# Kernel optimization log

Hardware: AMD Instinct MI355X
Metric: run time of the kernel (lower is better)

Reference implementation:

```python
import jax, jax.numpy as jnp
import numpy as np

N_NODES = 50000   # hypergraph nodes
N_EDGES = 20000   # hyperedges
M = 400000        # node-edge incidences (node copies)
L = 800000        # inner GIN graph edges per side
HID = 128
IN_DIM = 128
B = 32            # graphs in batch
C = 10            # num_classes
N_LAYERS = 2
INNER = 2         # inner_num_layers
BN_EPS = 1e-5


def setup_inputs() -> dict:
    key = jax.random.key(0)
    ks = jax.random.split(key, 16)
    s = 0.05
    inp = {}
    inp["x_N"] = jax.random.normal(ks[0], (N_NODES, IN_DIM), jnp.float32)
    # embedding linear
    inp["We"] = jax.random.normal(ks[1], (IN_DIM, HID), jnp.float32) * s
    inp["be"] = jnp.zeros((HID,), jnp.float32)
    # GIN params: [outer_layer, direction(N2E/E2N), inner_conv, mlp_linear, hid, hid]
    inp["Wg"] = jax.random.normal(ks[2], (N_LAYERS, 2, INNER, 2, HID, HID), jnp.float32) * s
    inp["bg"] = jnp.zeros((N_LAYERS, 2, INNER, 2, HID), jnp.float32)
    inp["eps_g"] = jnp.zeros((N_LAYERS, 2, INNER), jnp.float32)
    # eval-mode BatchNorm affine params per inner conv
    inp["gamma"] = jnp.ones((N_LAYERS, 2, INNER, HID), jnp.float32)
    inp["beta"] = jnp.zeros((N_LAYERS, 2, INNER, HID), jnp.float32)
    # per-layer prediction heads
    inp["Wp"] = jax.random.normal(ks[3], (N_LAYERS + 1, HID, C), jnp.float32) * s
    inp["bp"] = jnp.zeros((N_LAYERS + 1, C), jnp.float32)
    # index tensors
    inp["ori_node_idx"] = jax.random.randint(ks[4], (M,), 0, N_NODES)
    inp["node2edge"] = jax.random.randint(ks[5], (M,), 0, N_EDGES)
    inp["edge_index_N"] = jax.random.randint(ks[6], (2, L), 0, M)
    inp["ori_edge_idx"] = jax.random.randint(ks[7], (M,), 0, N_EDGES)
    inp["edge2node"] = jax.random.randint(ks[8], (M,), 0, N_NODES)
    inp["edge_index_E"] = jax.random.randint(ks[9], (2, L), 0, M)
    inp["batch"] = jax.random.randint(ks[10], (M,), 0, B)
    return inp


def _gin(x, src, dst, Wg, bg, eps, gamma, beta):
    # GIN over the copy graph: h = MLP((1+eps)*x + sum_{j->i} x_j), BN (eval), ReLU between convs
    inv_std = 1.0 / jnp.sqrt(1.0 + BN_EPS)
    n = x.shape[0]
    for l in range(INNER):
        agg = jax.ops.segment_sum(x[src], dst, num_segments=n)
        h = (1.0 + eps[l]) * x + agg
        h = jax.nn.relu(h @ Wg[l, 0] + bg[l, 0])
        h = h @ Wg[l, 1] + bg[l, 1]
        h = gamma[l] * h * inv_std + beta[l]
        x = jax.nn.relu(h) if l < INNER - 1 else h
    return x


def reference(x_N, We, be, Wg, bg, eps_g, gamma, beta, Wp, bp,
              ori_node_idx, node2edge, edge_index_N,
              ori_edge_idx, edge2node, edge_index_E, batch):
    node_x = x_N @ We + be                       # [N, HID]
    xs = [node_x]
    for i in range(N_LAYERS):
        # node -> edge: gather copies, inner GIN, segment-sum pool over hyperedges
        nx = node_x[ori_node_idx]                # [M, HID]
        nx = _gin(nx, edge_index_N[0], edge_index_N[1],
                  Wg[i, 0], bg[i, 0], eps_g[i, 0], gamma[i, 0], beta[i, 0])
        edge_x = jax.ops.segment_sum(nx, node2edge, num_segments=N_EDGES)
        edge_x = jax.nn.relu(edge_x)             # EdgeUpdate (dropout off in eval)
        # edge -> node
        ex = edge_x[ori_edge_idx]                # [M, HID]
        ex = _gin(ex, edge_index_E[0], edge_index_E[1],
                  Wg[i, 1], bg[i, 1], eps_g[i, 1], gamma[i, 1], beta[i, 1])
        node_x = jax.ops.segment_sum(ex, edge2node, num_segments=N_NODES)
        node_x = jax.nn.relu(node_x)             # NodeUpdate
        xs.append(node_x)
    score = jnp.zeros((B, C), x_N.dtype)
    for i, x in enumerate(xs):
        pooled = jax.ops.segment_sum(x[ori_node_idx], batch, num_segments=B)
        score = score + pooled @ Wp[i] + bp[i]
    return score
```

## Files before the change

### kernel.cpp

```cpp
#include <hip/hip_runtime.h>
#include <hip/hip_bf16.h>

#define HID 128
static const int N_NODES = 50000;
static const int N_EDGES = 20000;
static const int M_COPIES = 400000;
static const int L_EDGES = 800000;
static const int NBATCH = 32;
static const int NCLS = 10;
#define INV_STD 0.9999950000374997f
#define IDX_CAP 384
#define PKSHIFT 19
#define PKMASK  0x7FFFF

typedef __attribute__((ext_vector_type(4))) float f32x4;
typedef __attribute__((ext_vector_type(8))) short short8;
typedef __attribute__((ext_vector_type(8))) unsigned short ushort8;
typedef __attribute__((ext_vector_type(4))) unsigned short u16x4;

__device__ __forceinline__ float bf2f(unsigned short u) {
    union { unsigned u; float f; } v; v.u = ((unsigned)u) << 16; return v.f;
}
__device__ __forceinline__ unsigned short f2bf(float f) {
    union { float f; unsigned u; } v; v.f = f;
    unsigned r = v.u + 0x7FFFu + ((v.u >> 16) & 1u);
    return (unsigned short)(r >> 16);
}
__device__ __forceinline__ void gatomic_add(float* p, float v) {
    unsafeAtomicAdd(p, v);
}

__device__ __forceinline__ unsigned short* xs_addr(unsigned short* Xs, int c, int r) {
    int byte = ((c * 64 + r) * 16) ^ ((c & 7) << 4);
    return (unsigned short*)((char*)Xs + byte);
}

__device__ __forceinline__ void stage8(const unsigned short* __restrict__ Wmat, int e,
                                       unsigned short* buf, int wave, int lane) {
    const char* g = (const char*)Wmat + ((size_t)e << 12) + (wave << 10) + (lane << 4);
    char* l = (char*)buf + (wave << 10);
    __builtin_amdgcn_global_load_lds(
        (const __attribute__((address_space(1))) unsigned int*)g,
        (__attribute__((address_space(3))) unsigned int*)l,
        16, 0, 0);
}

template<int N>
__device__ __forceinline__ void pipe_barrier() {
    if constexpr (N == 0) asm volatile("s_waitcnt vmcnt(0)" ::: "memory");
    else                  asm volatile("s_waitcnt vmcnt(1)" ::: "memory");
    __builtin_amdgcn_s_barrier();
    asm volatile("" ::: "memory");
}

__device__ __forceinline__ void mfma4(const unsigned short* Ws, const short8* xv,
                                      f32x4& a, int quad, int ln) {
#pragma unroll
    for (int kc = 0; kc < 4; ++kc) {
        short8 wa = *(const short8*)(Ws + (((kc * 4 + quad) * 16) + ln) * 8);
        a = __builtin_amdgcn_mfma_f32_16x16x32_bf16(wa, xv[kc], a, 0, 0, 0);
    }
}

__global__ __launch_bounds__(256) void prep_w(const float* __restrict__ We,
                                              const float* __restrict__ Wg,
                                              unsigned short* __restrict__ Wt) {
    int t = blockIdx.x * 256 + threadIdx.x;
    if (t >= 17 * 16384) return;
    int mat = t >> 14, rem = t & 16383;
    int h = rem >> 11, r2 = rem & 2047;
    int gg = r2 >> 7, r3 = r2 & 127;
    int n = r3 >> 3, j = r3 & 7;
    int k = gg * 8 + j, col = h * 16 + n;
    const float* src = (mat == 0) ? We : (Wg + (size_t)(mat - 1) * 16384);
    Wt[t] = f2bf(src[k * 128 + col]);
}

__global__ __launch_bounds__(256) void hist2_k(
    const int* __restrict__ iA, int nA, int* __restrict__ cA,
    const int* __restrict__ iB, int nB, int* __restrict__ cB, int shift) {
    int t = blockIdx.x * 256 + threadIdx.x;
    if (t < nA) atomicAdd(&cA[iA[t] >> shift], 1);
    if (t < nB) atomicAdd(&cB[iB[t] >> shift], 1);
}

__global__ __launch_bounds__(256) void scan1d_k(
    int* __restrict__ a0, int n0, int* __restrict__ p0,
    int* __restrict__ a1, int n1, int* __restrict__ p1) {
    int* a    = blockIdx.y ? a1 : a0;
    int n     = blockIdx.y ? n1 : n0;
    int* part = blockIdx.y ? p1 : p0;
    if ((int)(blockIdx.x * 256) >= n) return;
    __shared__ int s[256];
    int i = blockIdx.x * 256 + threadIdx.x;
    int v = (i < n) ? a[i] : 0;
    s[threadIdx.x] = v;
    __syncthreads();
#pragma unroll
    for (int d = 1; d < 256; d <<= 1) {
        int t = (threadIdx.x >= d) ? s[threadIdx.x - d] : 0;
        __syncthreads();
        s[threadIdx.x] += t;
        __syncthreads();
    }
    if (i < n) a[i] = s[threadIdx.x] - v;
    if (threadIdx.x == 255) part[blockIdx.x] = s[255];
}

__global__ __launch_bounds__(256) void scan2d_k(
    int* __restrict__ p0, int nb0, int* __restrict__ p1, int nb1) {
    int* part = blockIdx.x ? p1 : p0;
    int nb    = blockIdx.x ? nb1 : nb0;
    __shared__ int s[256];
    __shared__ int carry;
    if (threadIdx.x == 0) carry = 0;
    __syncthreads();
    for (int base = 0; base < nb; base += 256) {
        int i = base + threadIdx.x;
        int v = (i < nb) ? part[i] : 0;
        s[threadIdx.x] = v;
        __syncthreads();
#pragma unroll
        for (int d = 1; d < 256; d <<= 1) {
            int t = (threadIdx.x >= d) ? s[threadIdx.x - d] : 0;
            __syncthreads();
            s[threadIdx.x] += t;
            __syncthreads();
        }
        if (i < nb) part[i] = carry + s[threadIdx.x] - v;
        __syncthreads();
        if (threadIdx.x == 0) carry += s[255];
        __syncthreads();
    }
}

__global__ __launch_bounds__(256) void scan3d_k(
    int* __restrict__ a0, int n0, const int* __restrict__ p0,
    int* __restrict__ a1, int n1, const int* __restrict__ p1) {
    int* a          = blockIdx.y ? a1 : a0;
    int n           = blockIdx.y ? n1 : n0;
    const int* part = blockIdx.y ? p1 : p0;
    int i = blockIdx.x * 256 + threadIdx.x;
    if (i < n) a[i] += part[blockIdx.x];
}

__global__ __launch_bounds__(256) void fill_edgeblk2_k(
    const int* __restrict__ sA, const int* __restrict__ dA, const int* __restrict__ rA,
    int nA, int* __restrict__ oA, int2* __restrict__ pkA,
    const int* __restrict__ sB, const int* __restrict__ dB, const int* __restrict__ rB,
    int nB, int* __restrict__ oB, int2* __restrict__ pkB) {
    int t = blockIdx.x * 256 + threadIdx.x;
    if (t < nA) {
        int d = dA[t]; int pos = atomicAdd(&oA[d >> 6], 1);
        int s = sA[t]; int rl = (d & 63) << PKSHIFT;
        pkA[pos] = (int2){rl | s, rl | rA[s]};
    }
    if (t < nB) {
        int d = dB[t]; int pos = atomicAdd(&oB[d >> 6], 1);
        int s = sB[t]; int rl = (d & 63) << PKSHIFT;
        pkB[pos] = (int2){rl | s, rl | rB[s]};
    }
}

__global__ __launch_bounds__(256) void fill_pool2_k(
    const int* __restrict__ gA, int nA, int* __restrict__ oA, int* __restrict__ rkA,
    const int* __restrict__ gB, int nB, int* __restrict__ oB, int* __restrict__ rkB) {
    int t = blockIdx.x * 256 + threadIdx.x;
    if (t < nA) rkA[t] = atomicAdd(&oA[gA[t]], 1);
    if (t < nB) rkB[t] = atomicAdd(&oB[gB[t]], 1);
}

template<bool PROJ>
__global__ __launch_bounds__(256) void segsum_pool(
    const unsigned short* __restrict__ tbl, const int* __restrict__ off,
    unsigned short* __restrict__ out, int nseg,
    const float* __restrict__ Wp, float* __restrict__ y)
{
    int wave = threadIdx.x >> 6, lane = threadIdx.x & 63;
    int seg = blockIdx.x * 4 + wave;
    if (seg >= nseg) return;
    int start = (seg == 0) ? 0 : off[seg - 1];
    int end = off[seg];
    int g = lane & 15, sub = lane >> 4;
    float a[8] = {0.f, 0.f, 0.f, 0.f, 0.f, 0.f, 0.f, 0.f};
    int p = start + sub;
    for (; p + 4 < end; p += 8) {
        ushort8 v0 = *(const ushort8*)(tbl + (size_t)p * 128 + g * 8);
        ushort8 v1 = *(const ushort8*)(tbl + (size_t)(p + 4) * 128 + g * 8);
#pragma unroll
        for (int j = 0; j < 8; ++j) a[j] += bf2f(v0[j]) + bf2f(v1[j]);
    }
    if (p < end) {
        ushort8 v = *(const ushort8*)(tbl + (size_t)p * 128 + g * 8);
#pragma unroll
        for (int j = 0; j < 8; ++j) a[j] += bf2f(v[j]);
    }
#pragma unroll
    for (int j = 0; j < 8; ++j) {
        a[j] += __shfl_xor(a[j], 16, 64);
        a[j] += __shfl_xor(a[j], 32, 64);
    }
    if (sub == 0) {
        float r[8];
        ushort8 ov;
#pragma unroll
        for (int j = 0; j < 8; ++j) { r[j] = fmaxf(a[j], 0.f); ov[j] = f2bf(r[j]); }
        *(ushort8*)(out + (size_t)seg * 128 + g * 8) = ov;
        if (PROJ) {
            float part[NCLS];
#pragma unroll
            for (int c = 0; c < NCLS; ++c) part[c] = 0.f;
#pragma unroll
            for (int j = 0; j < 8; ++j) {
                float xv = r[j];
                const float* w = Wp + (g * 8 + j) * NCLS;
#pragma unroll
                for (int c = 0; c < NCLS; ++c) part[c] += xv * w[c];
            }
#pragma unroll
            for (int d = 1; d < 16; d <<= 1)
#pragma unroll
                for (int c = 0; c < NCLS; ++c) part[c] += __shfl_xor(part[c], d, 64);
            if (g == 0) {
                float* yp = y + (size_t)seg * NCLS;
#pragma unroll
                for (int c = 0; c < NCLS; ++c) yp[c] += part[c];
            }
        }
    }
}

template<bool CONV0>
__global__ __launch_bounds__(256, 5) void fused_conv(
    const unsigned short* __restrict__ tbl,
    const int* __restrict__ self_idx,
    const int* __restrict__ blkOff, const int2* __restrict__ edgePk,
    const int* __restrict__ outIdx,
    const float* __restrict__ eps_ptr,
    const unsigned short* __restrict__ W1t, const float* __restrict__ b1,
    const unsigned short* __restrict__ W2t, const float* __restrict__ b2,
    const float* __restrict__ gam, const float* __restrict__ bet,
    unsigned short* __restrict__ out)
{
    __shared__ __align__(16) unsigned short Xs[16 * 64 * 8];
    __shared__ __align__(16) unsigned short Wsb[3][2048];
    __shared__ int sIdx[IDX_CAP];
    __shared__ int sSelf[64];
    __shared__ int rcnt[64], rbase[64], rpos[64];
    const int tid = threadIdx.x;
    const int row0 = blockIdx.x * 64;
    const int wave = tid >> 6, lane = tid & 63;

    stage8(W1t, 0, Wsb[0], wave, lane);
    stage8(W1t, 1, Wsb[1], wave, lane);

    const int blk = blockIdx.x;
    const int bstart = (blk == 0) ? 0 : blkOff[blk - 1];
    const int cnt = blkOff[blk] - bstart;

    if (tid < 64) sSelf[tid] = CONV0 ? self_idx[row0 + tid] : row0 + tid;
    __syncthreads();

    const float e = 1.0f + eps_ptr[0];
    const int g = tid & 15;
    const int rb = tid >> 4;
    float a[4][8];
#pragma unroll
    for (int i = 0; i < 4; ++i) {
        int self = sSelf[rb + 16 * i];
        ushort8 u = *(const ushort8*)(tbl + (size_t)self * 128 + g * 8);
#pragma unroll
        for (int j = 0; j < 8; ++j) a[i][j] = e * bf2f(u[j]);
    }

    int done = 0;
    while (done < cnt) {
        const int chunk = (cnt - done < IDX_CAP) ? (cnt - done) : IDX_CAP;
        if (tid < 64) rcnt[tid] = 0;
        __syncthreads();
        int e0 = -1, e1 = -1;
        if (tid < chunk) {
            int2 pk = edgePk[bstart + done + tid];
            e0 = CONV0 ? pk.y : pk.x;
            atomicAdd(&rcnt[e0 >> PKSHIFT], 1);
        }
        if (tid + 256 < chunk) {
            int2 pk = edgePk[bstart + done + tid + 256];
            e1 = CONV0 ? pk.y : pk.x;
            atomicAdd(&rcnt[e1 >> PKSHIFT], 1);
        }
        __syncthreads();
        if (tid < 64) {
            int c = rcnt[tid];
            int s = c;
#pragma unroll
            for (int d = 1; d < 64; d <<= 1) {
                int t = __shfl_up(s, d, 64);
                if (tid >= d) s += t;
            }
            rbase[tid] = s - c;
            rpos[tid]  = s - c;
        }
        __syncthreads();
        if (e0 >= 0) { int p = atomicAdd(&rpos[e0 >> PKSHIFT], 1); sIdx[p] = e0 & PKMASK; }
        if (e1 >= 0) { int p = atomicAdd(&rpos[e1 >> PKSHIFT], 1); sIdx[p] = e1 & PKMASK; }
        __syncthreads();

        int st[4], en[4];
#pragma unroll
        for (int i = 0; i < 4; ++i) {
            int r = rb + 16 * i;
            st[i] = rbase[r]; en[i] = rpos[r];
        }
        const int cmax = chunk - 1;
        while (__ballot((st[0] < en[0]) | (st[1] < en[1]) |
                        (st[2] < en[2]) | (st[3] < en[3]))) {
            ushort8 v[4];
#pragma unroll
            for (int i = 0; i < 4; ++i) {
                int p = st[i] < cmax ? st[i] : cmax;
                int idx = sIdx[p];
                v[i] = *(const ushort8*)(tbl + (size_t)idx * 128 + g * 8);
            }
#pragma unroll
            for (int i = 0; i < 4; ++i) {
                if (st[i] < en[i]) {
#pragma unroll
                    for (int j = 0; j < 8; ++j) a[i][j] += bf2f(v[i][j]);
                    st[i]++;
                }
            }
        }
        done += chunk;
        __syncthreads();
    }

#pragma unroll
    for (int i = 0; i < 4; ++i) {
        ushort8 xv;
#pragma unroll
        for (int j = 0; j < 8; ++j) xv[j] = f2bf(a[i][j]);
        *(ushort8*)xs_addr(Xs, g, rb + 16 * i) = xv;
    }
    __syncthreads();

    const int ln = lane & 15, quad = lane >> 4;
    const int row = wave * 16 + ln;

    short8 xb[4];
#pragma unroll
    for (int kc = 0; kc < 4; ++kc)
        xb[kc] = *(const short8*)xs_addr(Xs, kc * 4 + quad, row);

    f32x4 acc[8];
#pragma unroll
    for (int t = 0; t < 8; ++t) acc[t] = (f32x4){0.f, 0.f, 0.f, 0.f};

#pragma unroll
    for (int s = 0; s < 8; ++s) {
        int pf = s + 2;
        stage8(pf < 8 ? W1t : W2t, pf & 7, Wsb[pf % 3], wave, lane);
        mfma4(Wsb[s % 3], xb, acc[s], quad, ln);
        pipe_barrier<1>();
    }

    {
        const int j0 = (quad & 1) * 4;
#pragma unroll
        for (int t = 0; t < 8; ++t) {
            int p0 = t * 16 + quad * 4;
            f32x4 bv = *(const f32x4*)(b1 + p0);
            u16x4 hp;
#pragma unroll
            for (int i = 0; i < 4; ++i) hp[i] = f2bf(fmaxf(acc[t][i] + bv[i], 0.f));
            *(u16x4*)((char*)xs_addr(Xs, p0 >> 3, row) + j0 * 2) = hp;
        }
    }

    short8 hb[4];
#pragma unroll
    for (int kc = 0; kc < 4; ++kc)
        hb[kc] = *(const short8*)xs_addr(Xs, kc * 4 + quad, row);

#pragma unroll
    for (int t = 0; t < 8; ++t) acc[t] = (f32x4){0.f, 0.f, 0.f, 0.f};

#pragma unroll
    for (int f = 0; f < 8; ++f) {
        if (f < 6) stage8(W2t, f + 2, Wsb[(f + 10) % 3], wave, lane);
        mfma4(Wsb[(f + 8) % 3], hb, acc[f], quad, ln);
        if (f < 6)      pipe_barrier<1>();
        else if (f == 6) pipe_barrier<0>();
    }

    const int m = row0 + row;
    const int orow = CONV0 ? m : outIdx[m];
    unsigned short* obase = out + (size_t)orow * 128;
#pragma unroll
    for (int t = 0; t < 8; ++t) {
        int n0 = t * 16 + quad * 4;
        f32x4 bv = *(const f32x4*)(b2 + n0);
        f32x4 gv = *(const f32x4*)(gam + n0);
        f32x4 tv = *(const f32x4*)(bet + n0);
        u16x4 op;
#pragma unroll
        for (int i = 0; i < 4; ++i) {
            float h = acc[t][i] + bv[i];
            h = gv[i] * h * INV_STD + tv[i];
            if (CONV0) h = fmaxf(h, 0.f);
            op[i] = f2bf(h);
        }
        *(u16x4*)(obase + n0) = op;
    }
}

__global__ __launch_bounds__(256) void gemm_embed(
    const float* __restrict__ in, const unsigned short* __restrict__ Wt,
    const float* __restrict__ bias, unsigned short* __restrict__ out_bf, int rows)
{
    __shared__ __align__(16) unsigned short Xs[16 * 64 * 8];
    __shared__ __align__(16) unsigned short Ws[16 * 128 * 8];
    int tid = threadIdx.x;
    int row0 = blockIdx.x * 64;
#pragma unroll
    for (int i = 0; i < 8; ++i) {
        int chunk = tid + i * 256;
        int n = chunk >> 4, g = chunk & 15;
        *(short8*)(Ws + (g * 128 + n) * 8) =
            *(const short8*)(Wt + (n >> 4) * 2048 + g * 128 + (n & 15) * 8);
    }
#pragma unroll
    for (int i = 0; i < 4; ++i) {
        int chunk = tid + i * 256;
        int r = chunk >> 4, g = chunk & 15;
        int gr = row0 + r;
        ushort8 v;
        if (gr < rows) {
            const float* p = in + (size_t)gr * 128 + g * 8;
            f32x4 a0 = *(const f32x4*)p;
            f32x4 a1 = *(const f32x4*)(p + 4);
#pragma unroll
            for (int j = 0; j < 4; ++j) { v[j] = f2bf(a0[j]); v[4 + j] = f2bf(a1[j]); }
        } else {
#pragma unroll
            for (int j = 0; j < 8; ++j) v[j] = 0;
        }
        *(ushort8*)(Xs + (g * 64 + r) * 8) = v;
    }
    __syncthreads();
    int wave = tid >> 6, lane = tid & 63;
    int m0 = wave * 16;
    int ln = lane & 15, quad = lane >> 4;
    f32x4 acc[8];
#pragma unroll
    for (int t = 0; t < 8; ++t) acc[t] = (f32x4){0.f, 0.f, 0.f, 0.f};
#pragma unroll
    for (int kc = 0; kc < 4; ++kc) {
        int g = kc * 4 + quad;
        short8 a = *(const short8*)(Xs + (g * 64 + m0 + ln) * 8);
#pragma unroll
        for (int t = 0; t < 8; ++t) {
            short8 b = *(const short8*)(Ws + (g * 128 + t * 16 + ln) * 8);
            acc[t] = __builtin_amdgcn_mfma_f32_16x16x32_bf16(a, b, acc[t], 0, 0, 0);
        }
    }
#pragma unroll
    for (int t = 0; t < 8; ++t) {
        int col = t * 16 + ln;
        float bi = bias[col];
#pragma unroll
        for (int i = 0; i < 4; ++i) {
            int gr = row0 + m0 + quad * 4 + i;
            if (gr < rows) out_bf[(size_t)gr * 128 + col] = f2bf(acc[t][i] + bi);
        }
    }
}

__global__ __launch_bounds__(256) void proj_y0(
    const unsigned short* __restrict__ nx, const float* __restrict__ Wp,
    float* __restrict__ y, int rows)
{
    __shared__ float Wl[HID * NCLS];
    for (int i = threadIdx.x; i < HID * NCLS; i += 256) Wl[i] = Wp[i];
    __syncthreads();
    int r = blockIdx.x * 256 + threadIdx.x;
    if (r >= rows) return;
    float acc[NCLS];
#pragma unroll
    for (int c = 0; c < NCLS; ++c) acc[c] = 0.f;
    const unsigned short* xp = nx + (size_t)r * 128;
#pragma unroll 4
    for (int g = 0; g < 16; ++g) {
        ushort8 u = *(const ushort8*)(xp + g * 8);
#pragma unroll
        for (int j = 0; j < 8; ++j) {
            float xv = bf2f(u[j]);
            const float* w = Wl + (g * 8 + j) * NCLS;
#pragma unroll
            for (int c = 0; c < NCLS; ++c) acc[c] += xv * w[c];
        }
    }
    float* yp = y + (size_t)r * NCLS;
#pragma unroll
    for (int c = 0; c < NCLS; ++c) yp[c] = acc[c];
}

__global__ __launch_bounds__(256) void score_scatter(
    const float* __restrict__ y, const int* __restrict__ ori,
    const int* __restrict__ batch, float* __restrict__ score)
{
    __shared__ float sc[NBATCH * NCLS];
    for (int i = threadIdx.x; i < NBATCH * NCLS; i += 256) sc[i] = 0.f;
    __syncthreads();
    int stride = gridDim.x * 256;
    for (int m = blockIdx.x * 256 + threadIdx.x; m < M_COPIES; m += stride) {
        int r = ori[m], b = batch[m];
        const float* yp = y + (size_t)r * NCLS;
#pragma unroll
        for (int c = 0; c < NCLS; ++c)
            __hip_atomic_fetch_add(&sc[b * NCLS + c], yp[c],
                                   __ATOMIC_RELAXED, __HIP_MEMORY_SCOPE_WORKGROUP);
    }
    __syncthreads();
    for (int i = threadIdx.x; i < NBATCH * NCLS; i += 256) gatomic_add(score + i, sc[i]);
}

__global__ void score_final(const float* __restrict__ score, const float* __restrict__ bp,
                            float* __restrict__ out)
{
    int t = threadIdx.x;
    if (t >= NBATCH * NCLS) return;
    int c = t % NCLS;
    out[t] = score[t] + bp[c] + bp[NCLS + c] + bp[2 * NCLS + c];
}

__global__ void fill_sentinel(float* out, int n, float enc) {
    int t = blockIdx.x * 64 + threadIdx.x;
    if (t < n) out[t] = enc;
}

extern "C" void kernel_launch(void* const* d_in, const int* in_sizes, int n_in,
                              void* d_out, int out_size, void* d_ws, size_t ws_size,
                              hipStream_t stream) {
    const float* x_N    = (const float*)d_in[0];
    const float* We     = (const float*)d_in[1];
    const float* be     = (const float*)d_in[2];
    const float* Wg     = (const float*)d_in[3];
    const float* bg     = (const float*)d_in[4];
    const float* eps_g  = (const float*)d_in[5];
    const float* gam    = (const float*)d_in[6];
    const float* bet    = (const float*)d_in[7];
    const float* Wp     = (const float*)d_in[8];
    const float* bp     = (const float*)d_in[9];
    const int* ori_node = (const int*)d_in[10];
    const int* node2edge= (const int*)d_in[11];
    const int* eiN      = (const int*)d_in[12];
    const int* ori_edge = (const int*)d_in[13];
    const int* edge2node= (const int*)d_in[14];
    const int* eiE      = (const int*)d_in[15];
    const int* batch    = (const int*)d_in[16];

    const int NBLK = M_COPIES / 64;

    char* p = (char*)d_ws;
    auto take = [&](size_t n) { char* r = p; p += (n + 255) & ~(size_t)255; return r; };
    unsigned short* Wt  = (unsigned short*)take((size_t)17 * 16384 * 2);
    unsigned short* Xb  = (unsigned short*)take((size_t)M_COPIES * 128 * 2);
    unsigned short* Xb2 = (unsigned short*)take((size_t)M_COPIES * 128 * 2);
    unsigned short* nx  = (unsigned short*)take((size_t)N_NODES * 128 * 2);
    unsigned short* ex  = (unsigned short*)take((size_t)N_EDGES * 128 * 2);
    float* y            = (float*)take((size_t)N_NODES * NCLS * 4);
    float* score        = (float*)take((size_t)NBATCH * NCLS * 4);
    int* blkN           = (int*)take((size_t)2 * NBLK * 4);
    int* blkE           = blkN + NBLK;
    int* off_n2e        = (int*)take((size_t)N_EDGES * 4);
    int* off_e2n        = (int*)take((size_t)N_NODES * 4);
    int2* pkN           = (int2*)take((size_t)L_EDGES * 8);
    int2* pkE           = (int2*)take((size_t)L_EDGES * 8);
    int* rk_n2e         = (int*)take((size_t)M_COPIES * 4);
    int* rk_e2n         = (int*)take((size_t)M_COPIES * 4);
    int* part           = (int*)take((size_t)8192 * 4);
    size_t need = (size_t)(p - (char*)d_ws);
    if (need > ws_size) {
        fill_sentinel<<<(out_size + 63) / 64, 64, 0, stream>>>(
            (float*)d_out, out_size, 1.0e9f + (float)ws_size);
        return;
    }

    prep_w<<<1088, 256, 0, stream>>>(We, Wg, Wt);
    (void)hipMemsetAsync(score, 0, (size_t)NBATCH * NCLS * 4, stream);

    const int NB_M = (M_COPIES + 255) / 256;
    const int NB_L = (L_EDGES + 255) / 256;
    const int NB_N = (N_NODES + 255) / 256;
    const int NB_B = (NBLK + 255) / 256;
    int* partB = part + 4096;

    (void)hipMemsetAsync(blkN, 0, (size_t)2 * NBLK * 4, stream);
    hist2_k<<<NB_L, 256, 0, stream>>>(eiN + L_EDGES, L_EDGES, blkN,
                                      eiE + L_EDGES, L_EDGES, blkE, 6);
    scan1d_k<<<dim3(NB_B, 2), 256, 0, stream>>>(blkN, NBLK, part, blkE, NBLK, partB);
    scan2d_k<<<2, 256, 0, stream>>>(part, NB_B, partB, NB_B);
    scan3d_k<<<dim3(NB_B, 2), 256, 0, stream>>>(blkN, NBLK, part, blkE, NBLK, partB);
    fill_edgeblk2_k<<<NB_L, 256, 0, stream>>>(
        eiN, eiN + L_EDGES, ori_node, L_EDGES, blkN, pkN,
        eiE, eiE + L_EDGES, ori_edge, L_EDGES, blkE, pkE);

    (void)hipMemsetAsync(off_n2e, 0,
        (size_t)((char*)off_e2n - (char*)off_n2e) + (size_t)N_NODES * 4, stream);
    hist2_k<<<NB_M, 256, 0, stream>>>(node2edge, M_COPIES, off_n2e,
                                      edge2node, M_COPIES, off_e2n, 0);
    scan1d_k<<<dim3(NB_N, 2), 256, 0, stream>>>(off_n2e, N_EDGES, part, off_e2n, N_NODES, partB);
    scan2d_k<<<2, 256, 0, stream>>>(part, (N_EDGES + 255) / 256, partB, NB_N);
    scan3d_k<<<dim3(NB_N, 2), 256, 0, stream>>>(off_n2e, N_EDGES, part, off_e2n, N_NODES, partB);
    fill_pool2_k<<<NB_M, 256, 0, stream>>>(node2edge, M_COPIES, off_n2e, rk_n2e,
                                           edge2node, M_COPIES, off_e2n, rk_e2n);

    gemm_embed<<<(N_NODES + 63) / 64, 256, 0, stream>>>(x_N, Wt, be, nx, N_NODES);
    proj_y0<<<(N_NODES + 255) / 256, 256, 0, stream>>>(nx, Wp, y, N_NODES);

    for (int layer = 0; layer < 2; ++layer) {
        for (int dir = 0; dir < 2; ++dir) {
            int cj0 = layer * 4 + dir * 2;
            int cj1 = cj0 + 1;
            const unsigned short* base = (dir == 0) ? nx : ex;
            const int* selfI = (dir == 0) ? ori_node : ori_edge;
            const int* blkD  = (dir == 0) ? blkN : blkE;
            const int2* pkD  = (dir == 0) ? pkN : pkE;
            const int* rkD   = (dir == 0) ? rk_n2e : rk_e2n;

            fused_conv<true><<<NBLK, 256, 0, stream>>>(
                base, selfI, blkD, pkD, nullptr, eps_g + cj0,
                Wt + (size_t)(1 + cj0 * 2) * 16384, bg + (cj0 * 2) * 128,
                Wt + (size_t)(1 + cj0 * 2 + 1) * 16384, bg + (cj0 * 2 + 1) * 128,
                gam + cj0 * 128, bet + cj0 * 128, Xb);
            fused_conv<false><<<NBLK, 256, 0, stream>>>(
                Xb, nullptr, blkD, pkD, rkD, eps_g + cj1,
                Wt + (size_t)(1 + cj1 * 2) * 16384, bg + (cj1 * 2) * 128,
                Wt + (size_t)(1 + cj1 * 2 + 1) * 16384, bg + (cj1 * 2 + 1) * 128,
                gam + cj1 * 128, bet + cj1 * 128, Xb2);
            if (dir == 0) {
                segsum_pool<false><<<(N_EDGES + 3) / 4, 256, 0, stream>>>(
                    Xb2, off_n2e, ex, N_EDGES, nullptr, nullptr);
            } else {
                segsum_pool<true><<<(N_NODES + 3) / 4, 256, 0, stream>>>(
                    Xb2, off_e2n, nx, N_NODES,
                    Wp + (size_t)(layer + 1) * HID * NCLS, y);
            }
        }
    }
    score_scatter<<<256, 256, 0, stream>>>(y, ori_node, batch, score);
    score_final<<<1, 320, 0, stream>>>(score, bp, (float*)d_out);
}
```

Before: 1.412 ms.

## Merge index preprocessing kernels and gather pooled rows via item lists

Fuses the two histogram passes and the two fill passes into single kernels. The block-offset scan now runs as one scan2d call instead of three, and all offset buffers are cleared with one memset. The second GIN conv now writes rows in copy order instead of scattering them through a rank permutation. Segment pooling instead gathers rows through a per-segment item list built during the fill pass. The fused_conv aggregation also accumulates as packed float2 pairs, which may allow packed FP32 math. These changes aim to cut launch overhead and scattered writes, at the cost of an extra indirection load in the pooling kernels.

```diff
diff --git a/kernel.cpp b/kernel.cpp
--- a/kernel.cpp
+++ b/kernel.cpp
@@ -14,6 +14,7 @@
 #define PKMASK  0x7FFFF
 
 typedef __attribute__((ext_vector_type(4))) float f32x4;
+typedef __attribute__((ext_vector_type(2))) float f32x2;
 typedef __attribute__((ext_vector_type(8))) short short8;
 typedef __attribute__((ext_vector_type(8))) unsigned short ushort8;
 typedef __attribute__((ext_vector_type(4))) unsigned short u16x4;
@@ -28,6 +29,12 @@
 }
 __device__ __forceinline__ void gatomic_add(float* p, float v) {
     unsafeAtomicAdd(p, v);
+}
+__device__ __forceinline__ f32x2 bf2x2(unsigned w) {
+    union { unsigned x; float y; } lo, hi;
+    lo.x = w << 16; hi.x = w & 0xFFFF0000u;
+    f32x2 f; f[0] = lo.y; f[1] = hi.y;
+    return f;
 }
 
 __device__ __forceinline__ unsigned short* xs_addr(unsigned short* Xs, int c, int r) {
@@ -76,12 +83,20 @@
     Wt[t] = f2bf(src[k * 128 + col]);
 }
 
-__global__ __launch_bounds__(256) void hist2_k(
-    const int* __restrict__ iA, int nA, int* __restrict__ cA,
-    const int* __restrict__ iB, int nB, int* __restrict__ cB, int shift) {
+__global__ __launch_bounds__(256) void hist4_k(
+    const int* __restrict__ dEN, const int* __restrict__ dEE, int L,
+    int* __restrict__ cN, int* __restrict__ cE,
+    const int* __restrict__ gN, const int* __restrict__ gE, int M,
+    int* __restrict__ oN, int* __restrict__ oE) {
     int t = blockIdx.x * 256 + threadIdx.x;
-    if (t < nA) atomicAdd(&cA[iA[t] >> shift], 1);
-    if (t < nB) atomicAdd(&cB[iB[t] >> shift], 1);
+    if (t < L) {
+        atomicAdd(&cN[dEN[t] >> 6], 1);
+        atomicAdd(&cE[dEE[t] >> 6], 1);
+    }
+    if (t < M) {
+        atomicAdd(&oN[gN[t]], 1);
+        atomicAdd(&oE[gE[t]], 1);
+    }
 }
 
 __global__ __launch_bounds__(256) void scan1d_k(
@@ -144,36 +159,37 @@
     if (i < n) a[i] += part[blockIdx.x];
 }
 
-__global__ __launch_bounds__(256) void fill_edgeblk2_k(
+__global__ __launch_bounds__(256) void fill4_k(
     const int* __restrict__ sA, const int* __restrict__ dA, const int* __restrict__ rA,
-    int nA, int* __restrict__ oA, int2* __restrict__ pkA,
+    int L, int* __restrict__ oA, int2* __restrict__ pkA,
     const int* __restrict__ sB, const int* __restrict__ dB, const int* __restrict__ rB,
-    int nB, int* __restrict__ oB, int2* __restrict__ pkB) {
+    int* __restrict__ oB, int2* __restrict__ pkB,
+    const int* __restrict__ gA, const int* __restrict__ gB, int M,
+    int* __restrict__ pA, int* __restrict__ itA,
+    int* __restrict__ pB, int* __restrict__ itB) {
     int t = blockIdx.x * 256 + threadIdx.x;
-    if (t < nA) {
-        int d = dA[t]; int pos = atomicAdd(&oA[d >> 6], 1);
-        int s = sA[t]; int rl = (d & 63) << PKSHIFT;
-        pkA[pos] = (int2){rl | s, rl | rA[s]};
-    }
-    if (t < nB) {
-        int d = dB[t]; int pos = atomicAdd(&oB[d >> 6], 1);
-        int s = sB[t]; int rl = (d & 63) << PKSHIFT;
-        pkB[pos] = (int2){rl | s, rl | rB[s]};
-    }
-}
-
-__global__ __launch_bounds__(256) void fill_pool2_k(
-    const int* __restrict__ gA, int nA, int* __restrict__ oA, int* __restrict__ rkA,
-    const int* __restrict__ gB, int nB, int* __restrict__ oB, int* __restrict__ rkB) {
-    int t = blockIdx.x * 256 + threadIdx.x;
-    if (t < nA) rkA[t] = atomicAdd(&oA[gA[t]], 1);
-    if (t < nB) rkB[t] = atomicAdd(&oB[gB[t]], 1);
+    if (t < L) {
+        {
+            int d = dA[t]; int pos = atomicAdd(&oA[d >> 6], 1);
+            int s = sA[t]; int rl = (d & 63) << PKSHIFT;
+            pkA[pos] = (int2){rl | s, rl | rA[s]};
+        }
+        {
+            int d = dB[t]; int pos = atomicAdd(&oB[d >> 6], 1);
+            int s = sB[t]; int rl = (d & 63) << PKSHIFT;
+            pkB[pos] = (int2){rl | s, rl | rB[s]};
+        }
+    }
+    if (t < M) {
+        { int pos = atomicAdd(&pA[gA[t]], 1); itA[pos] = t; }
+        { int pos = atomicAdd(&pB[gB[t]], 1); itB[pos] = t; }
+    }
 }
 
 template<bool PROJ>
 __global__ __launch_bounds__(256) void segsum_pool(
     const unsigned short* __restrict__ tbl, const int* __restrict__ off,
-    unsigned short* __restrict__ out, int nseg,
+    const int* __restrict__ items, unsigned short* __restrict__ out, int nseg,
     const float* __restrict__ Wp, float* __restrict__ y)
 {
     int wave = threadIdx.x >> 6, lane = threadIdx.x & 63;
@@ -185,13 +201,15 @@
     float a[8] = {0.f, 0.f, 0.f, 0.f, 0.f, 0.f, 0.f, 0.f};
     int p = start + sub;
     for (; p + 4 < end; p += 8) {
-        ushort8 v0 = *(const ushort8*)(tbl + (size_t)p * 128 + g * 8);
-        ushort8 v1 = *(const ushort8*)(tbl + (size_t)(p + 4) * 128 + g * 8);
+        int r0 = items[p], r1 = items[p + 4];
+        ushort8 v0 = *(const ushort8*)(tbl + (size_t)r0 * 128 + g * 8);
+        ushort8 v1 = *(const ushort8*)(tbl + (size_t)r1 * 128 + g * 8);
 #pragma unroll
         for (int j = 0; j < 8; ++j) a[j] += bf2f(v0[j]) + bf2f(v1[j]);
     }
     if (p < end) {
-        ushort8 v = *(const ushort8*)(tbl + (size_t)p * 128 + g * 8);
+        int r = items[p];
+        ushort8 v = *(const ushort8*)(tbl + (size_t)r * 128 + g * 8);
 #pragma unroll
         for (int j = 0; j < 8; ++j) a[j] += bf2f(v[j]);
     }
@@ -235,7 +253,6 @@
     const unsigned short* __restrict__ tbl,
     const int* __restrict__ self_idx,
     const int* __restrict__ blkOff, const int2* __restrict__ edgePk,
-    const int* __restrict__ outIdx,
     const float* __restrict__ eps_ptr,
     const unsigned short* __restrict__ W1t, const float* __restrict__ b1,
     const unsigned short* __restrict__ W2t, const float* __restrict__ b2,
@@ -264,13 +281,14 @@
     const float e = 1.0f + eps_ptr[0];
     const int g = tid & 15;
     const int rb = tid >> 4;
-    float a[4][8];
+    f32x2 a[4][4];
 #pragma unroll
     for (int i = 0; i < 4; ++i) {
         int self = sSelf[rb + 16 * i];
         ushort8 u = *(const ushort8*)(tbl + (size_t)self * 128 + g * 8);
-#pragma unroll
-        for (int j = 0; j < 8; ++j) a[i][j] = e * bf2f(u[j]);
+        const unsigned* du = (const unsigned*)&u;
+#pragma unroll
+        for (int q = 0; q < 4; ++q) a[i][q] = bf2x2(du[q]) * e;
     }
 
     int done = 0;
@@ -325,8 +343,9 @@
 #pragma unroll
             for (int i = 0; i < 4; ++i) {
                 if (st[i] < en[i]) {
-#pragma unroll
-                    for (int j = 0; j < 8; ++j) a[i][j] += bf2f(v[i][j]);
+                    const unsigned* dv = (const unsigned*)&v[i];
+#pragma unroll
+                    for (int q = 0; q < 4; ++q) a[i][q] += bf2x2(dv[q]);
                     st[i]++;
                 }
             }
@@ -339,7 +358,10 @@
     for (int i = 0; i < 4; ++i) {
         ushort8 xv;
 #pragma unroll
-        for (int j = 0; j < 8; ++j) xv[j] = f2bf(a[i][j]);
+        for (int q = 0; q < 4; ++q) {
+            xv[2 * q]     = f2bf(a[i][q][0]);
+            xv[2 * q + 1] = f2bf(a[i][q][1]);
+        }
         *(ushort8*)xs_addr(Xs, g, rb + 16 * i) = xv;
     }
     __syncthreads();
@@ -394,8 +416,6 @@
     }
 
     const int m = row0 + row;
-    const int orow = CONV0 ? m : outIdx[m];
-    unsigned short* obase = out + (size_t)orow * 128;
 #pragma unroll
     for (int t = 0; t < 8; ++t) {
         int n0 = t * 16 + quad * 4;
@@ -410,7 +430,7 @@
             if (CONV0) h = fmaxf(h, 0.f);
             op[i] = f2bf(h);
         }
-        *(u16x4*)(obase + n0) = op;
+        *(u16x4*)(out + (size_t)m * 128 + n0) = op;
     }
 }
 
@@ -571,14 +591,15 @@
     unsigned short* ex  = (unsigned short*)take((size_t)N_EDGES * 128 * 2);
     float* y            = (float*)take((size_t)N_NODES * NCLS * 4);
     float* score        = (float*)take((size_t)NBATCH * NCLS * 4);
-    int* blkN           = (int*)take((size_t)2 * NBLK * 4);
+    int* offs           = (int*)take((size_t)(2 * NBLK + N_EDGES + N_NODES) * 4);
+    int* blkN           = offs;
     int* blkE           = blkN + NBLK;
-    int* off_n2e        = (int*)take((size_t)N_EDGES * 4);
-    int* off_e2n        = (int*)take((size_t)N_NODES * 4);
+    int* off_n2e        = blkE + NBLK;
+    int* off_e2n        = off_n2e + N_EDGES;
     int2* pkN           = (int2*)take((size_t)L_EDGES * 8);
     int2* pkE           = (int2*)take((size_t)L_EDGES * 8);
-    int* rk_n2e         = (int*)take((size_t)M_COPIES * 4);
-    int* rk_e2n         = (int*)take((size_t)M_COPIES * 4);
+    int* it_n2e         = (int*)take((size_t)M_COPIES * 4);
+    int* it_e2n         = (int*)take((size_t)M_COPIES * 4);
     int* part           = (int*)take((size_t)8192 * 4);
     size_t need = (size_t)(p - (char*)d_ws);
     if (need > ws_size) {
@@ -590,31 +611,22 @@
     prep_w<<<1088, 256, 0, stream>>>(We, Wg, Wt);
     (void)hipMemsetAsync(score, 0, (size_t)NBATCH * NCLS * 4, stream);
 
-    const int NB_M = (M_COPIES + 255) / 256;
     const int NB_L = (L_EDGES + 255) / 256;
     const int NB_N = (N_NODES + 255) / 256;
-    const int NB_B = (NBLK + 255) / 256;
     int* partB = part + 4096;
 
-    (void)hipMemsetAsync(blkN, 0, (size_t)2 * NBLK * 4, stream);
-    hist2_k<<<NB_L, 256, 0, stream>>>(eiN + L_EDGES, L_EDGES, blkN,
-                                      eiE + L_EDGES, L_EDGES, blkE, 6);
-    scan1d_k<<<dim3(NB_B, 2), 256, 0, stream>>>(blkN, NBLK, part, blkE, NBLK, partB);
-    scan2d_k<<<2, 256, 0, stream>>>(part, NB_B, partB, NB_B);
-    scan3d_k<<<dim3(NB_B, 2), 256, 0, stream>>>(blkN, NBLK, part, blkE, NBLK, partB);
-    fill_edgeblk2_k<<<NB_L, 256, 0, stream>>>(
-        eiN, eiN + L_EDGES, ori_node, L_EDGES, blkN, pkN,
-        eiE, eiE + L_EDGES, ori_edge, L_EDGES, blkE, pkE);
-
-    (void)hipMemsetAsync(off_n2e, 0,
-        (size_t)((char*)off_e2n - (char*)off_n2e) + (size_t)N_NODES * 4, stream);
-    hist2_k<<<NB_M, 256, 0, stream>>>(node2edge, M_COPIES, off_n2e,
-                                      edge2node, M_COPIES, off_e2n, 0);
+    (void)hipMemsetAsync(offs, 0, (size_t)(2 * NBLK + N_EDGES + N_NODES) * 4, stream);
+    hist4_k<<<NB_L, 256, 0, stream>>>(
+        eiN + L_EDGES, eiE + L_EDGES, L_EDGES, blkN, blkE,
+        node2edge, edge2node, M_COPIES, off_n2e, off_e2n);
+    scan2d_k<<<2, 256, 0, stream>>>(blkN, NBLK, blkE, NBLK);
     scan1d_k<<<dim3(NB_N, 2), 256, 0, stream>>>(off_n2e, N_EDGES, part, off_e2n, N_NODES, partB);
     scan2d_k<<<2, 256, 0, stream>>>(part, (N_EDGES + 255) / 256, partB, NB_N);
     scan3d_k<<<dim3(NB_N, 2), 256, 0, stream>>>(off_n2e, N_EDGES, part, off_e2n, N_NODES, partB);
-    fill_pool2_k<<<NB_M, 256, 0, stream>>>(node2edge, M_COPIES, off_n2e, rk_n2e,
-                                           edge2node, M_COPIES, off_e2n, rk_e2n);
+    fill4_k<<<NB_L, 256, 0, stream>>>(
+        eiN, eiN + L_EDGES, ori_node, L_EDGES, blkN, pkN,
+        eiE, eiE + L_EDGES, ori_edge, blkE, pkE,
+        node2edge, edge2node, M_COPIES, off_n2e, it_n2e, off_e2n, it_e2n);
 
     gemm_embed<<<(N_NODES + 63) / 64, 256, 0, stream>>>(x_N, Wt, be, nx, N_NODES);
     proj_y0<<<(N_NODES + 255) / 256, 256, 0, stream>>>(nx, Wp, y, N_NODES);
@@ -627,24 +639,23 @@
             const int* selfI = (dir == 0) ? ori_node : ori_edge;
             const int* blkD  = (dir == 0) ? blkN : blkE;
             const int2* pkD  = (dir == 0) ? pkN : pkE;
-            const int* rkD   = (dir == 0) ? rk_n2e : rk_e2n;
 
             fused_conv<true><<<NBLK, 256, 0, stream>>>(
-                base, selfI, blkD, pkD, nullptr, eps_g + cj0,
+                base, selfI, blkD, pkD, eps_g + cj0,
                 Wt + (size_t)(1 + cj0 * 2) * 16384, bg + (cj0 * 2) * 128,
                 Wt + (size_t)(1 + cj0 * 2 + 1) * 16384, bg + (cj0 * 2 + 1) * 128,
                 gam + cj0 * 128, bet + cj0 * 128, Xb);
             fused_conv<false><<<NBLK, 256, 0, stream>>>(
-                Xb, nullptr, blkD, pkD, rkD, eps_g + cj1,
+                Xb, nullptr, blkD, pkD, eps_g + cj1,
                 Wt + (size_t)(1 + cj1 * 2) * 16384, bg + (cj1 * 2) * 128,
                 Wt + (size_t)(1 + cj1 * 2 + 1) * 16384, bg + (cj1 * 2 + 1) * 128,
                 gam + cj1 * 128, bet + cj1 * 128, Xb2);
             if (dir == 0) {
                 segsum_pool<false><<<(N_EDGES + 3) / 4, 256, 0, stream>>>(
-                    Xb2, off_n2e, ex, N_EDGES, nullptr, nullptr);
+                    Xb2, off_n2e, it_n2e, ex, N_EDGES, nullptr, nullptr);
             } else {
                 segsum_pool<true><<<(N_NODES + 3) / 4, 256, 0, stream>>>(
-                    Xb2, off_e2n, nx, N_NODES,
+                    Xb2, off_e2n, it_e2n, nx, N_NODES,
                     Wp + (size_t)(layer + 1) * HID * NCLS, y);
             }
         }
```

Result: no change. 1.402 ms (-0.7%).
